# Kernel tuning notes

Measured on AMD Instinct MI355X. Metric: run time of the kernel, lower is better.

Reference implementation:

```python
import jax, jax.numpy as jnp
import numpy as np

N_NODES = 50000


def setup_inputs() -> dict:
    key = jax.random.key(0)
    k1, k2, k3, k4 = jax.random.split(key, 4)
    in_dim, out_dim, n_edges = 128, 64, 800000
    x = jax.random.normal(k1, (N_NODES, in_dim), dtype=jnp.float32)
    edge_index = jax.random.randint(k2, (2, n_edges), 0, N_NODES, dtype=jnp.int64)
    W = jax.random.normal(k3, (in_dim, out_dim), dtype=jnp.float32) * (1.0 / np.sqrt(in_dim))
    att = jax.random.normal(k4, (2 * out_dim,), dtype=jnp.float32) * (1.0 / np.sqrt(2 * out_dim))
    return {"x": x, "edge_index": edge_index, "W": W, "att": att}


def reference(x, edge_index, W, att):
    N = x.shape[0]
    F_out = W.shape[1]
    h = x @ W                                   # [N, F]
    src, dst = edge_index[0], edge_index[1]
    hs = h[src]                                 # [E, F] gather
    hd = h[dst]                                 # [E, F] gather
    # att(cat([h_src, h_dst])) == h_src @ a1 + h_dst @ a2
    a1, a2 = att[:F_out], att[F_out:]
    logit = jax.nn.leaky_relu(hs @ a1 + hd @ a2, 0.2)   # [E]
    E = logit.shape[0]
    # The original builds a dense [N, E] matrix (row d holds logit_e at col e
    # for dst[e]==d, zeros elsewhere) and softmaxes over the E axis. The
    # equivalent sparse form: denom_d = sum_{e:dst=d} exp(logit_e) + (E - deg_d)*exp(0),
    # stabilized with m_d = max(max logit over segment, 0).
    seg_max = jax.ops.segment_max(logit, dst, num_segments=N)      # -inf on empty
    m = jnp.maximum(seg_max, 0.0)                                  # include the zero cells
    exp_l = jnp.exp(logit - m[dst])                                # [E]
    seg_sum = jax.ops.segment_sum(exp_l, dst, num_segments=N)      # [N]
    deg = jax.ops.segment_sum(jnp.ones_like(logit), dst, num_segments=N)
    denom = seg_sum + (jnp.float32(E) - deg) * jnp.exp(-m)         # zeros' contribution
    w = exp_l / denom[dst]                                          # [E]
    agg = jax.ops.segment_sum(w[:, None] * hs, dst, num_segments=N)  # [N, F]
    return jax.nn.elu(agg)
```

## Files before the change

### kernel.cpp

```cpp
#include <hip/hip_runtime.h>
#include <hip/hip_bf16.h>

#define FIN 128
#define FOUT 64
#define BINW 128
#define NBINPAD 512
#define QS 2560
#define TILE 2048
#define DPQ 32
#define RCAP 768

typedef __attribute__((ext_vector_type(8))) short short8;
typedef __attribute__((ext_vector_type(4))) float f32x4;

__device__ __forceinline__ unsigned short f2bf(float f) {
    unsigned u = __float_as_uint(f);
    unsigned r = u + 0x7FFFu + ((u >> 16) & 1u);
    return (unsigned short)(r >> 16);
}

__device__ __forceinline__ float f16lo(unsigned u) {
    return (float)__builtin_bit_cast(_Float16, (unsigned short)(u & 0xFFFFu));
}
__device__ __forceinline__ float f16hi(unsigned u) {
    return (float)__builtin_bit_cast(_Float16, (unsigned short)(u >> 16));
}

__global__ __launch_bounds__(256) void k_prep(
    const float* __restrict__ W,
    unsigned short* __restrict__ Whig, unsigned short* __restrict__ Wlog,
    int* __restrict__ qcur, int nzero)
{
    const int t = threadIdx.x;
    if (blockIdx.x >= 64) {
        const int i = (blockIdx.x - 64) * 256 + t;
        if (i < nzero) qcur[i] = 0;
        return;
    }
    const int f = blockIdx.x * 256 + t;
    const int combo = f >> 9;
    const int s = combo >> 2, c = combo & 3;
    const int r = f & 511;
    const int l = r >> 3, j = r & 7;
    const int k = s * 32 + (l >> 4) * 8 + j;
    const int n = c * 16 + (l & 15);
    const float w = W[k * 64 + n];
    const unsigned short hi = f2bf(w);
    const float hif = __uint_as_float((unsigned)hi << 16);
    Whig[f] = hi;
    Wlog[f] = f2bf(w - hif);
}

__global__ __launch_bounds__(256, 8) void k_fused(
    const float* __restrict__ x, const unsigned short* __restrict__ Whig,
    const unsigned short* __restrict__ Wlog, const float* __restrict__ att,
    unsigned* __restrict__ h2, float* __restrict__ as_, float* __restrict__ ad_,
    const int* __restrict__ src, const int* __restrict__ dst,
    unsigned* __restrict__ queue, int* __restrict__ qcur,
    int N, int E, int nbins, int paBlocks)
{
    union SMem {
        struct { unsigned rec[TILE]; unsigned rec2[TILE];
                 int hist[NBINPAD]; int comb[NBINPAD]; int wtot[4]; } pa;
    };
    __shared__ SMem sm;
    const int t = threadIdx.x;

    if ((int)blockIdx.x < paBlocks) {
        const int e0 = blockIdx.x * TILE;
        const int tot = (E - e0 < TILE) ? (E - e0) : TILE;
        const int wv = t >> 6, lane = t & 63;

        sm.pa.hist[t] = 0; sm.pa.hist[t + 256] = 0;
        __syncthreads();

        if (tot == TILE) {
            const int4* dp = (const int4*)(dst + e0);
            const int4* sp = (const int4*)(src + e0);
            #pragma unroll
            for (int i = 0; i < TILE / 1024; ++i) {
                const int4 dv = dp[i * 256 + t];
                const int4 sv = sp[i * 256 + t];
                const int idx = (i * 256 + t) * 4;
                sm.pa.rec[idx + 0] = (unsigned)sv.x | ((unsigned)dv.x << 16);
                sm.pa.rec[idx + 1] = (unsigned)sv.y | ((unsigned)dv.y << 16);
                sm.pa.rec[idx + 2] = (unsigned)sv.z | ((unsigned)dv.z << 16);
                sm.pa.rec[idx + 3] = (unsigned)sv.w | ((unsigned)dv.w << 16);
                atomicAdd(&sm.pa.hist[dv.x >> 7], 1);
                atomicAdd(&sm.pa.hist[dv.y >> 7], 1);
                atomicAdd(&sm.pa.hist[dv.z >> 7], 1);
                atomicAdd(&sm.pa.hist[dv.w >> 7], 1);
            }
        } else {
            #pragma unroll
            for (int i = 0; i < TILE / 256; ++i) {
                const int idx = i * 256 + t;
                const int e = e0 + idx;
                if (e < E) {
                    const int d = __builtin_nontemporal_load(dst + e);
                    const int s = __builtin_nontemporal_load(src + e);
                    sm.pa.rec[idx] = (unsigned)s | ((unsigned)d << 16);
                    atomicAdd(&sm.pa.hist[d >> 7], 1);
                }
            }
        }
        __syncthreads();

        const int b0 = 2 * t;
        const int v0 = sm.pa.hist[b0], v1 = sm.pa.hist[b0 + 1];
        const int tv = v0 + v1;
        int sc = tv;
        #pragma unroll
        for (int off = 1; off < 64; off <<= 1) {
            const int nb = __shfl_up(sc, off);
            if (lane >= off) sc += nb;
        }
        if (lane == 63) sm.pa.wtot[wv] = sc;
        __syncthreads();
        int wbase = 0;
        #pragma unroll
        for (int w = 0; w < 4; ++w) wbase += (w < wv) ? sm.pa.wtot[w] : 0;
        const int ex0 = wbase + (sc - tv);
        const int ex1 = ex0 + v0;
        int c0 = 0, c1 = 0;
        if (b0 < nbins && v0 > 0)
            c0 = b0 * QS + atomicAdd(qcur + b0, v0) - ex0;
        if (b0 + 1 < nbins && v1 > 0)
            c1 = (b0 + 1) * QS + atomicAdd(qcur + b0 + 1, v1) - ex1;
        sm.pa.hist[b0] = ex0; sm.pa.hist[b0 + 1] = ex1;
        sm.pa.comb[b0] = c0;  sm.pa.comb[b0 + 1] = c1;
        __syncthreads();

        #pragma unroll
        for (int i = 0; i < TILE / 256; ++i) {
            const int idx = i * 256 + t;
            if (idx < tot) {
                const unsigned r = sm.pa.rec[idx];
                const int b = (int)(r >> 23);
                const int pos = atomicAdd(&sm.pa.hist[b], 1);
                sm.pa.rec2[pos] = r;
            }
        }
        __syncthreads();

        for (int idx = t; idx < tot; idx += 256) {
            const unsigned r = sm.pa.rec2[idx];
            const int b = (int)(r >> 23);
            const int gpos = sm.pa.comb[b] + idx;
            if (gpos < (b + 1) * QS)
                __builtin_nontemporal_store(r, queue + gpos);
        }
        return;
    }

    const int bb = blockIdx.x - paBlocks;
    const int wv = t >> 6, lane = t & 63;
    const int quad = lane >> 4, mrow = lane & 15;
    const int r0 = (bb * 4 + wv) * 16;
    const int arow = r0 + mrow;
    const bool rok = arow < N;

    f32x4 acc[4] = {};

    #pragma unroll
    for (int s = 0; s < 4; ++s) {
        float xv[8];
        if (rok) {
            const float4* p = (const float4*)(x + (size_t)arow * FIN + s * 32 + quad * 8);
            const float4 u0 = p[0], u1 = p[1];
            xv[0] = u0.x; xv[1] = u0.y; xv[2] = u0.z; xv[3] = u0.w;
            xv[4] = u1.x; xv[5] = u1.y; xv[6] = u1.z; xv[7] = u1.w;
        } else {
            #pragma unroll
            for (int j = 0; j < 8; ++j) xv[j] = 0.f;
        }
        short8 ah, al;
        #pragma unroll
        for (int j = 0; j < 8; ++j) {
            const unsigned short hi = f2bf(xv[j]);
            const float hif = __uint_as_float((unsigned)hi << 16);
            ah[j] = (short)hi;
            al[j] = (short)f2bf(xv[j] - hif);
        }
        #pragma unroll
        for (int c = 0; c < 4; ++c) {
            const short8 bh = *(const short8*)&Whig[((s * 4 + c) * 64 + lane) * 8];
            const short8 bl = *(const short8*)&Wlog[((s * 4 + c) * 64 + lane) * 8];
            acc[c] = __builtin_amdgcn_mfma_f32_16x16x32_bf16(ah, bh, acc[c], 0, 0, 0);
            acc[c] = __builtin_amdgcn_mfma_f32_16x16x32_bf16(al, bh, acc[c], 0, 0, 0);
            acc[c] = __builtin_amdgcn_mfma_f32_16x16x32_bf16(ah, bl, acc[c], 0, 0, 0);
        }
    }

    float a1v[4], a2v[4];
    #pragma unroll
    for (int c = 0; c < 4; ++c) {
        a1v[c] = att[c * 16 + mrow];
        a2v[c] = att[64 + c * 16 + mrow];
    }
    #pragma unroll
    for (int reg = 0; reg < 4; ++reg) {
        float pa = 0.f, pb = 0.f;
        #pragma unroll
        for (int c = 0; c < 4; ++c) {
            pa = fmaf(acc[c][reg], a1v[c], pa);
            pb = fmaf(acc[c][reg], a2v[c], pb);
        }
        #pragma unroll
        for (int off = 1; off < 16; off <<= 1) {
            pa += __shfl_xor(pa, off);
            pb += __shfl_xor(pb, off);
        }
        const int orow = r0 + quad * 4 + reg;
        if (mrow == 0 && orow < N) {
            as_[orow] = pa;
            ad_[orow] = pb;
        }
    }

    #pragma unroll
    for (int reg = 0; reg < 4; ++reg) {
        const int orow = r0 + quad * 4 + reg;
        if (orow < N) {
            #pragma unroll
            for (int c = 0; c < 2; ++c) {
                const unsigned lo = (unsigned)__builtin_bit_cast(unsigned short,
                                        (_Float16)acc[c][reg]);
                const unsigned hi = (unsigned)__builtin_bit_cast(unsigned short,
                                        (_Float16)acc[c + 2][reg]);
                h2[(size_t)orow * 32 + c * 16 + mrow] = lo | (hi << 16);
            }
        }
    }
}

__global__ __launch_bounds__(256) void k_aggq(
    const int* __restrict__ qcur, const unsigned* __restrict__ queue,
    const float* __restrict__ as_, const float* __restrict__ ad_,
    const unsigned* __restrict__ h2, float* __restrict__ out,
    int N, float Ef)
{
    __shared__ unsigned rec[RCAP];
    __shared__ unsigned pay[RCAP];
    __shared__ float wexp[RCAP];
    __shared__ int hist[DPQ], base[DPQ], cur[DPQ];
    __shared__ float adl[DPQ];
    __shared__ int nloc;

    const int bin = blockIdx.x >> 2, q = blockIdx.x & 3;
    const int d0 = bin * BINW + q * DPQ;
    const int t = threadIdx.x;
    const int wv = t >> 6, lane = t & 63;

    if (t < DPQ) {
        hist[t] = 0;
        const int d = d0 + t;
        adl[t] = (d < N) ? ad_[d] : 0.f;
    }
    if (t == 0) nloc = 0;
    __syncthreads();

    int cnt = qcur[bin];
    if (cnt > QS) cnt = QS;

    for (int i = t; i < cnt; i += 256) {
        const unsigned r = __builtin_nontemporal_load(queue + (size_t)bin * QS + i);
        const bool m = ((int)((r >> 21) & 3) == q);
        const unsigned long long mk = __ballot(m);
        int b0 = 0;
        if (lane == 0 && mk) b0 = atomicAdd(&nloc, __popcll(mk));
        b0 = __shfl(b0, 0);
        if (m) {
            const int p = b0 + __popcll(mk & ((1ull << lane) - 1ull));
            if (p < RCAP) {
                rec[p] = r;
                atomicAdd(&hist[(r >> 16) & (DPQ - 1)], 1);
            }
        }
    }
    __syncthreads();
    int n = nloc; if (n > RCAP) n = RCAP;

    if (t < DPQ) base[t] = hist[t];
    __syncthreads();
    #pragma unroll
    for (int off = 1; off < DPQ; off <<= 1) {
        const int a = (t < DPQ && t >= off) ? base[t - off] : 0;
        __syncthreads();
        if (t < DPQ) base[t] += a;
        __syncthreads();
    }
    if (t < DPQ) { base[t] -= hist[t]; cur[t] = base[t]; }
    __syncthreads();

    for (int i = t; i < n; i += 256) {
        const unsigned r = rec[i];
        const int s  = (int)(r & 0xFFFFu);
        const int dl = (int)(r >> 16) & (DPQ - 1);
        const float z = as_[s] + adl[dl];
        const float lg = (z >= 0.f) ? z : 0.2f * z;
        const int pos = atomicAdd(&cur[dl], 1);
        pay[pos] = (unsigned)s;
        wexp[pos] = expf(lg);
    }
    __syncthreads();

    const int grp = lane >> 4, ln = lane & 15;
    const int g16 = wv * 4 + grp;
    #pragma unroll
    for (int k = 0; k < 2; ++k) {
        const int dl = g16 + k * 16;
        const int d = d0 + dl;
        const bool ok = (d < N);
        const int dg = ok ? hist[dl] : 0;
        const int bs = ok ? base[dl] : 0;

        float ss = 0.f;
        for (int j = ln; j < dg; j += 16) ss += wexp[bs + j];
        ss += __shfl_xor(ss, 8, 16);
        ss += __shfl_xor(ss, 4, 16);
        ss += __shfl_xor(ss, 2, 16);
        ss += __shfl_xor(ss, 1, 16);
        const float inv = 1.f / (ss + (Ef - (float)dg));

        float a00 = 0.f, a01 = 0.f, a10 = 0.f, a11 = 0.f;
        for (int jb = 0; jb < dg; jb += 8) {
            float w[8]; int s[8];
            #pragma unroll
            for (int u = 0; u < 8; ++u) {
                const int j = jb + u;
                if (j < dg) {
                    s[u] = (int)pay[bs + j];
                    w[u] = wexp[bs + j] * inv;
                } else { s[u] = 0; w[u] = 0.f; }
            }
            #pragma unroll
            for (int u = 0; u < 8; ++u) {
                const uint2 hp = *(const uint2*)&h2[(size_t)s[u] * 32 + 2 * ln];
                a00 += w[u] * f16lo(hp.x);
                a01 += w[u] * f16hi(hp.x);
                a10 += w[u] * f16lo(hp.y);
                a11 += w[u] * f16hi(hp.y);
            }
        }

        if (ok) {
            const float r00 = (a00 > 0.f) ? a00 : expm1f(a00);
            const float r10 = (a10 > 0.f) ? a10 : expm1f(a10);
            const float r01 = (a01 > 0.f) ? a01 : expm1f(a01);
            const float r11 = (a11 > 0.f) ? a11 : expm1f(a11);
            float2* op0 = (float2*)(out + (size_t)d * FOUT + 2 * ln);
            float2* op1 = (float2*)(out + (size_t)d * FOUT + 32 + 2 * ln);
            *op0 = make_float2(r00, r10);
            *op1 = make_float2(r01, r11);
        }
    }
}

extern "C" void kernel_launch(void* const* d_in, const int* in_sizes, int n_in,
                              void* d_out, int out_size, void* d_ws, size_t ws_size,
                              hipStream_t stream) {
    const float* x   = (const float*)d_in[0];
    const int*   ei  = (const int*)d_in[1];
    const float* W   = (const float*)d_in[2];
    const float* att = (const float*)d_in[3];

    const int N = in_sizes[0] / FIN;
    const int E = in_sizes[1] / 2;
    const int* src = ei;
    const int* dst = ei + E;

    const int NBINS = (N + BINW - 1) / BINW;

    char* ws = (char*)d_ws;
    size_t o = 0;
    auto carve = [&](size_t bytes) {
        void* p = ws + o; o += (bytes + 1023) & ~(size_t)1023; return p;
    };
    unsigned short* Whig = (unsigned short*)carve(16384 * 2);
    unsigned short* Wlog = (unsigned short*)carve(16384 * 2);
    float*          as_  = (float*)carve((size_t)N * 4);
    float*          ad_  = (float*)carve((size_t)N * 4);
    int*            qcur = (int*)carve((size_t)NBINS * 4);
    unsigned*       h2   = (unsigned*)carve((size_t)N * 32 * 4);
    unsigned*       queue = (unsigned*)carve((size_t)NBINS * QS * 4);

    float* out = (float*)d_out;

    const int paBlocks = (E + TILE - 1) / TILE;
    const int mmBlocks = (N + 63) / 64;
    const int zBlks    = (NBINS + 255) / 256;

    k_prep<<<64 + zBlks, 256, 0, stream>>>(W, Whig, Wlog, qcur, NBINS);
    k_fused<<<paBlocks + mmBlocks, 256, 0, stream>>>(
        x, Whig, Wlog, att, h2, as_, ad_, src, dst, queue, qcur, N, E, NBINS, paBlocks);
    k_aggq<<<NBINS * 4, 256, 0, stream>>>(qcur, queue, as_, ad_, h2, out, N, (float)E);
}
```

Before: 126.5 us.

## Split each bin across two aggregation blocks instead of four

Each aggregation block now handles 64 destination nodes (half a bin) instead of 32, so every bin's queue is scanned by two blocks rather than four. This halves the redundant global reads and filtering of queue records. The multi-barrier shared-memory prefix scan is replaced with a single-wavefront shuffle scan over 64 entries. In exchange, each block holds more records in shared memory (a larger cap) and does twice the per-destination aggregation work, and half as many blocks are launched.

```diff
diff --git a/kernel.cpp b/kernel.cpp
--- a/kernel.cpp
+++ b/kernel.cpp
@@ -7,8 +7,8 @@
 #define NBINPAD 512
 #define QS 2560
 #define TILE 2048
-#define DPQ 32
-#define RCAP 768
+#define DPH 64
+#define RCAPH 1408
 
 typedef __attribute__((ext_vector_type(8))) short short8;
 typedef __attribute__((ext_vector_type(4))) float f32x4;
@@ -240,19 +240,19 @@
     const unsigned* __restrict__ h2, float* __restrict__ out,
     int N, float Ef)
 {
-    __shared__ unsigned rec[RCAP];
-    __shared__ unsigned pay[RCAP];
-    __shared__ float wexp[RCAP];
-    __shared__ int hist[DPQ], base[DPQ], cur[DPQ];
-    __shared__ float adl[DPQ];
+    __shared__ unsigned rec[RCAPH];
+    __shared__ unsigned pay[RCAPH];
+    __shared__ float wexp[RCAPH];
+    __shared__ int hist[DPH], base[DPH], cur[DPH];
+    __shared__ float adl[DPH];
     __shared__ int nloc;
 
-    const int bin = blockIdx.x >> 2, q = blockIdx.x & 3;
-    const int d0 = bin * BINW + q * DPQ;
+    const int bin = blockIdx.x >> 1, half = blockIdx.x & 1;
+    const int d0 = bin * BINW + half * DPH;
     const int t = threadIdx.x;
     const int wv = t >> 6, lane = t & 63;
 
-    if (t < DPQ) {
+    if (t < DPH) {
         hist[t] = 0;
         const int d = d0 + t;
         adl[t] = (d < N) ? ad_[d] : 0.f;
@@ -265,38 +265,39 @@
 
     for (int i = t; i < cnt; i += 256) {
         const unsigned r = __builtin_nontemporal_load(queue + (size_t)bin * QS + i);
-        const bool m = ((int)((r >> 21) & 3) == q);
+        const bool m = (((r >> 22) & 1u) == (unsigned)half);
         const unsigned long long mk = __ballot(m);
         int b0 = 0;
         if (lane == 0 && mk) b0 = atomicAdd(&nloc, __popcll(mk));
         b0 = __shfl(b0, 0);
         if (m) {
             const int p = b0 + __popcll(mk & ((1ull << lane) - 1ull));
-            if (p < RCAP) {
+            if (p < RCAPH) {
                 rec[p] = r;
-                atomicAdd(&hist[(r >> 16) & (DPQ - 1)], 1);
+                atomicAdd(&hist[(r >> 16) & (DPH - 1)], 1);
             }
         }
     }
     __syncthreads();
-    int n = nloc; if (n > RCAP) n = RCAP;
-
-    if (t < DPQ) base[t] = hist[t];
-    __syncthreads();
-    #pragma unroll
-    for (int off = 1; off < DPQ; off <<= 1) {
-        const int a = (t < DPQ && t >= off) ? base[t - off] : 0;
-        __syncthreads();
-        if (t < DPQ) base[t] += a;
-        __syncthreads();
-    }
-    if (t < DPQ) { base[t] -= hist[t]; cur[t] = base[t]; }
+    int n = nloc; if (n > RCAPH) n = RCAPH;
+
+    if (wv == 0) {
+        const int v = hist[lane];
+        int sc = v;
+        #pragma unroll
+        for (int off = 1; off < 64; off <<= 1) {
+            const int nb = __shfl_up(sc, off);
+            if (lane >= off) sc += nb;
+        }
+        base[lane] = sc - v;
+        cur[lane] = sc - v;
+    }
     __syncthreads();
 
     for (int i = t; i < n; i += 256) {
         const unsigned r = rec[i];
         const int s  = (int)(r & 0xFFFFu);
-        const int dl = (int)(r >> 16) & (DPQ - 1);
+        const int dl = (int)(r >> 16) & (DPH - 1);
         const float z = as_[s] + adl[dl];
         const float lg = (z >= 0.f) ? z : 0.2f * z;
         const int pos = atomicAdd(&cur[dl], 1);
@@ -308,7 +309,7 @@
     const int grp = lane >> 4, ln = lane & 15;
     const int g16 = wv * 4 + grp;
     #pragma unroll
-    for (int k = 0; k < 2; ++k) {
+    for (int k = 0; k < 4; ++k) {
         const int dl = g16 + k * 16;
         const int d = d0 + dl;
         const bool ok = (d < N);
@@ -394,5 +395,5 @@
     k_prep<<<64 + zBlks, 256, 0, stream>>>(W, Whig, Wlog, qcur, NBINS);
     k_fused<<<paBlocks + mmBlocks, 256, 0, stream>>>(
         x, Whig, Wlog, att, h2, as_, ad_, src, dst, queue, qcur, N, E, NBINS, paBlocks);
-    k_aggq<<<NBINS * 4, 256, 0, stream>>>(qcur, queue, as_, ad_, h2, out, N, (float)E);
-}
+    k_aggq<<<NBINS * 2, 256, 0, stream>>>(qcur, queue, as_, ad_, h2, out, N, (float)E);
+}
```

New measurement: 131.3 us. 3.8% more time.

## Make queue accesses cache-friendly and vectorize bin scans with block remapping

Applied to the files above, without the earlier changes.

The partition writes to the queue now use ordinary stores instead of nontemporal ones, so the data can stay in cache for the aggregation kernel. Aggregation blocks are remapped so that the four quarter-blocks reading the same bin run close together in launch order, which raises the chance that a bin's queue is still cached when its siblings read it. The bin scan now loads four records per thread with uint4 vector loads and issues one shared atomic per wave per iteration instead of one per 64 records. The risks are reading past cnt within the QS-sized bin allocation, which is in bounds but reads stale data, and extra padded blocks that exit early.

```diff
diff --git a/kernel.cpp b/kernel.cpp
--- a/kernel.cpp
+++ b/kernel.cpp
@@ -148,7 +148,7 @@
             const int b = (int)(r >> 23);
             const int gpos = sm.pa.comb[b] + idx;
             if (gpos < (b + 1) * QS)
-                __builtin_nontemporal_store(r, queue + gpos);
+                queue[gpos] = r;
         }
         return;
     }
@@ -247,7 +247,12 @@
     __shared__ float adl[DPQ];
     __shared__ int nloc;
 
-    const int bin = blockIdx.x >> 2, q = blockIdx.x & 3;
+    const int nbins = (N + BINW - 1) / BINW;
+    const int f = blockIdx.x;
+    const int bin = ((f >> 5) << 3) + (f & 7);
+    const int q = (f >> 3) & 3;
+    if (bin >= nbins) return;
+
     const int d0 = bin * BINW + q * DPQ;
     const int t = threadIdx.x;
     const int wv = t >> 6, lane = t & 63;
@@ -263,20 +268,32 @@
     int cnt = qcur[bin];
     if (cnt > QS) cnt = QS;
 
-    for (int i = t; i < cnt; i += 256) {
-        const unsigned r = __builtin_nontemporal_load(queue + (size_t)bin * QS + i);
-        const bool m = ((int)((r >> 21) & 3) == q);
-        const unsigned long long mk = __ballot(m);
+    const unsigned* qb = queue + (size_t)bin * QS;
+    const unsigned long long below = (1ull << lane) - 1ull;
+    for (int base4 = 0; base4 < cnt; base4 += 1024) {
+        const int i4 = base4 + t * 4;
+        const uint4 r4 = *(const uint4*)(qb + i4);
+        const bool m0 = (i4 + 0 < cnt) && (((r4.x >> 21) & 3u) == (unsigned)q);
+        const bool m1 = (i4 + 1 < cnt) && (((r4.y >> 21) & 3u) == (unsigned)q);
+        const bool m2 = (i4 + 2 < cnt) && (((r4.z >> 21) & 3u) == (unsigned)q);
+        const bool m3 = (i4 + 3 < cnt) && (((r4.w >> 21) & 3u) == (unsigned)q);
+        const unsigned long long k0 = __ballot(m0), k1 = __ballot(m1);
+        const unsigned long long k2 = __ballot(m2), k3 = __ballot(m3);
+        const int tot = __popcll(k0) + __popcll(k1) + __popcll(k2) + __popcll(k3);
         int b0 = 0;
-        if (lane == 0 && mk) b0 = atomicAdd(&nloc, __popcll(mk));
+        if (lane == 0 && tot) b0 = atomicAdd(&nloc, tot);
         b0 = __shfl(b0, 0);
-        if (m) {
-            const int p = b0 + __popcll(mk & ((1ull << lane) - 1ull));
-            if (p < RCAP) {
-                rec[p] = r;
-                atomicAdd(&hist[(r >> 16) & (DPQ - 1)], 1);
-            }
-        }
+        const int b1 = b0 + __popcll(k0);
+        const int b2 = b1 + __popcll(k1);
+        const int b3 = b2 + __popcll(k2);
+        if (m0) { const int p = b0 + __popcll(k0 & below);
+            if (p < RCAP) { rec[p] = r4.x; atomicAdd(&hist[(r4.x >> 16) & (DPQ - 1)], 1); } }
+        if (m1) { const int p = b1 + __popcll(k1 & below);
+            if (p < RCAP) { rec[p] = r4.y; atomicAdd(&hist[(r4.y >> 16) & (DPQ - 1)], 1); } }
+        if (m2) { const int p = b2 + __popcll(k2 & below);
+            if (p < RCAP) { rec[p] = r4.z; atomicAdd(&hist[(r4.z >> 16) & (DPQ - 1)], 1); } }
+        if (m3) { const int p = b3 + __popcll(k3 & below);
+            if (p < RCAP) { rec[p] = r4.w; atomicAdd(&hist[(r4.w >> 16) & (DPQ - 1)], 1); } }
     }
     __syncthreads();
     int n = nloc; if (n > RCAP) n = RCAP;
@@ -390,9 +407,10 @@
     const int paBlocks = (E + TILE - 1) / TILE;
     const int mmBlocks = (N + 63) / 64;
     const int zBlks    = (NBINS + 255) / 256;
+    const int aggBlks  = ((NBINS + 7) / 8) * 32;
 
     k_prep<<<64 + zBlks, 256, 0, stream>>>(W, Whig, Wlog, qcur, NBINS);
     k_fused<<<paBlocks + mmBlocks, 256, 0, stream>>>(
         x, Whig, Wlog, att, h2, as_, ad_, src, dst, queue, qcur, N, E, NBINS, paBlocks);
-    k_aggq<<<NBINS * 4, 256, 0, stream>>>(qcur, queue, as_, ad_, h2, out, N, (float)E);
-}
+    k_aggq<<<aggBlks, 256, 0, stream>>>(qcur, queue, as_, ad_, h2, out, N, (float)E);
+}
```

Measured after the change: 124.4 us (median of 2 runs). No clear change (-1.7%).
